# Performance work log

Measured on AMD Instinct MI355X. Metric: run time of the kernel, lower is better.

Reference implementation:

```python
import jax, jax.numpy as jnp
import numpy as np

N = 100000
E = 1600000
H = 2   # heads
C = 64  # per-head channels
NEG_SLOPE = 0.2


def setup_inputs() -> dict:
    key = jax.random.key(0)
    ks = jax.random.split(key, 12)
    s = 0.05
    return {
        "logits": jax.random.normal(ks[0], (N, 40), jnp.float32),
        "features": jax.random.normal(ks[1], (N, 256), jnp.float32),
        "edge_index": jax.random.randint(ks[2], (2, E), 0, N, jnp.int32),
        "W_feat": jax.random.normal(ks[3], (256, 128), jnp.float32) * s,
        "b_feat": jnp.zeros((128,), jnp.float32),
        "W0": jax.random.normal(ks[4], (168, 128), jnp.float32) * s,
        "att_src0": jax.random.normal(ks[5], (H, C), jnp.float32) * s,
        "att_dst0": jax.random.normal(ks[6], (H, C), jnp.float32) * s,
        "bias0": jnp.zeros((128,), jnp.float32),
        "W1": jax.random.normal(ks[7], (128, 128), jnp.float32) * s,
        "att_src1": jax.random.normal(ks[8], (H, C), jnp.float32) * s,
        "att_dst1": jax.random.normal(ks[9], (H, C), jnp.float32) * s,
        "bias1": jnp.zeros((128,), jnp.float32),
        "W_out": jax.random.normal(ks[10], (128, 40), jnp.float32) * s,
        "b_out": jnp.zeros((40,), jnp.float32),
    }


def gat_conv(x, src, dst, W, att_src, att_dst, bias):
    # x: [N, F_in] -> h: [N, H, C]
    h = (x @ W).reshape(N, H, C)
    a_src = (h * att_src).sum(-1)  # [N, H]
    a_dst = (h * att_dst).sum(-1)  # [N, H]
    # per-edge attention logits, leaky relu
    e = jax.nn.leaky_relu(a_src[src] + a_dst[dst], NEG_SLOPE)  # [E+N, H]
    # segment softmax over incoming edges of each dst node
    e_max = jax.ops.segment_max(e, dst, num_segments=N)
    e_exp = jnp.exp(e - e_max[dst])
    denom = jax.ops.segment_sum(e_exp, dst, num_segments=N)
    alpha = e_exp / (denom[dst] + 1e-16)  # [E+N, H]
    # weighted message aggregation (scatter-add)
    msg = h[src] * alpha[:, :, None]  # [E+N, H, C]
    out = jax.ops.segment_sum(msg, dst, num_segments=N)
    return out.reshape(N, H * C) + bias


def reference(logits, features, edge_index, W_feat, b_feat,
              W0, att_src0, att_dst0, bias0,
              W1, att_src1, att_dst1, bias1,
              W_out, b_out):
    # input assembly: [logits | proj(features)]
    x = jnp.concatenate([logits, features @ W_feat + b_feat], axis=-1)  # [N,168]
    # add self loops (PyG GATConv default add_self_loops=True)
    loops = jnp.arange(N, dtype=edge_index.dtype)
    src = jnp.concatenate([edge_index[0], loops])
    dst = jnp.concatenate([edge_index[1], loops])
    x = gat_conv(x, src, dst, W0, att_src0, att_dst0, bias0)
    x = jax.nn.relu(x)  # relu between conv layers (dropout=0 / eval)
    x = gat_conv(x, src, dst, W1, att_src1, att_dst1, bias1)
    return x @ W_out + b_out  # [N, 40]
```

## Files before the change

### kernel.cpp

```cpp
#include <hip/hip_runtime.h>

#define NN 100000
#define EE 1600000
#define NBUCK ((NN + 255) >> 8)
#define CHUNK 8192
#define NPBLK ((EE + CHUNK - 1) / CHUNK)

typedef __attribute__((ext_vector_type(8))) short short8_t;
typedef __attribute__((ext_vector_type(4))) float f32x4;

static __device__ inline unsigned short f2bf(float f) {
    unsigned int u = __float_as_uint(f);
    u += 0x7FFFu + ((u >> 16) & 1u);
    return (unsigned short)(u >> 16);
}
static __device__ inline float bf2f(unsigned short h) {
    return __uint_as_float(((unsigned int)h) << 16);
}
static __device__ inline float u2f(unsigned int u) { return __uint_as_float(u); }

__global__ __launch_bounds__(256) void part_count(const int* __restrict__ ei,
                                                  int* __restrict__ cnt) {
    __shared__ int h[NBUCK];
    for (int i = threadIdx.x; i < NBUCK; i += 256) h[i] = 0;
    __syncthreads();
    int e0 = blockIdx.x * CHUNK;
    int e1 = e0 + CHUNK; if (e1 > EE) e1 = EE;
    for (int e = e0 + threadIdx.x; e < e1; e += 256)
        atomicAdd(&h[ei[EE + e] >> 8], 1);
    __syncthreads();
    for (int i = threadIdx.x; i < NBUCK; i += 256)
        cnt[blockIdx.x * NBUCK + i] = h[i];
}

__global__ void part_scan(const int* __restrict__ cnt, int* __restrict__ base,
                          int* __restrict__ bbase) {
    __shared__ int tot[512];
    int b = threadIdx.x;
    int t = 0;
    if (b < NBUCK)
        for (int k = 0; k < NPBLK; ++k) t += cnt[k * NBUCK + b];
    tot[b] = t;
    __syncthreads();
    for (int off = 1; off < 512; off <<= 1) {
        int u = (b >= off) ? tot[b - off] : 0;
        __syncthreads();
        tot[b] += u;
        __syncthreads();
    }
    int excl = tot[b] - t;
    if (b < NBUCK) {
        bbase[b] = excl;
        int run = excl;
        for (int k = 0; k < NPBLK; ++k) {
            base[k * NBUCK + b] = run;
            run += cnt[k * NBUCK + b];
        }
    }
    if (b == 0) bbase[NBUCK] = EE;
}

__global__ __launch_bounds__(256) void part_scatter(const int* __restrict__ ei,
                                                    const int* __restrict__ base,
                                                    unsigned int* __restrict__ bbuf) {
    __shared__ int lcur[NBUCK];
    for (int i = threadIdx.x; i < NBUCK; i += 256)
        lcur[i] = base[blockIdx.x * NBUCK + i];
    __syncthreads();
    int e0 = blockIdx.x * CHUNK;
    int e1 = e0 + CHUNK; if (e1 > EE) e1 = EE;
    for (int e = e0 + threadIdx.x; e < e1; e += 256) {
        int s = ei[e], d = ei[EE + e];
        int pos = atomicAdd(&lcur[d >> 8], 1);
        bbuf[pos] = (unsigned int)s | ((unsigned int)(d & 255) << 24);
    }
}

__global__ __launch_bounds__(256) void csr_build(const unsigned int* __restrict__ bbuf,
                                                 const int* __restrict__ bbase,
                                                 int* __restrict__ row_ptr,
                                                 int* __restrict__ col) {
    __shared__ int hist[256];
    __shared__ int sc[256];
    __shared__ int lcur[256];
    int b = blockIdx.x;
    int t = threadIdx.x;
    int n0 = b << 8;
    int nCnt = NN - n0; if (nCnt > 256) nCnt = 256;
    int es = bbase[b], ee2 = bbase[b + 1];
    hist[t] = 0;
    __syncthreads();
    for (int i = es + t; i < ee2; i += 256)
        atomicAdd(&hist[bbuf[i] >> 24], 1);
    __syncthreads();
    int v = hist[t];
    sc[t] = v;
    __syncthreads();
    for (int off = 1; off < 256; off <<= 1) {
        int u = (t >= off) ? sc[t - off] : 0;
        __syncthreads();
        sc[t] += u;
        __syncthreads();
    }
    int excl = sc[t] - v;
    if (t < nCnt) row_ptr[n0 + t] = es + excl;
    if (b == 0 && t == 0) row_ptr[NN] = EE;
    lcur[t] = excl;
    __syncthreads();
    for (int i = es + t; i < ee2; i += 256) {
        unsigned int pk = bbuf[i];
        int lpos = atomicAdd(&lcur[pk >> 24], 1);
        col[es + lpos] = (int)(pk & 0x00FFFFFFu);
    }
}

__global__ void bsplit_kernel(const float* __restrict__ W, int ldw, int K, int N,
                              unsigned short* __restrict__ BThi,
                              unsigned short* __restrict__ BTlo,
                              int stride, int koff, int KPseg) {
    int k = blockIdx.x * 256 + threadIdx.x;
    int col = blockIdx.y;
    if (k >= KPseg) return;
    float v = (k < K && col < N) ? W[(size_t)k * ldw + col] : 0.f;
    unsigned short hi = f2bf(v);
    unsigned short lo = f2bf(v - bf2f(hi));
    BThi[(size_t)col * stride + koff + k] = hi;
    BTlo[(size_t)col * stride + koff + k] = lo;
}

__global__ void cvec_kernel(const float* __restrict__ b_feat,
                            const float* __restrict__ W0, float* __restrict__ cvec) {
    int j = threadIdx.x;
    float s = 0.f;
    for (int k = 0; k < 128; ++k) s += b_feat[k] * W0[(40 + k) * 128 + j];
    cvec[j] = s;
}

template <int OUTBF16, int AMODE, int ATTN, int NCT>
__global__ __launch_bounds__(256) void mfma_gemm_kernel(
    const void* __restrict__ A1v, int lda1, int K1, int KP1,
    const float* __restrict__ A2, int lda2, int K2,
    int M,
    const unsigned short* __restrict__ BThi, const unsigned short* __restrict__ BTlo,
    int bstride, int KPtot,
    void* __restrict__ Cout, int ldc, int Nact, const float* __restrict__ bias,
    const float* __restrict__ att_src, const float* __restrict__ att_dst,
    float* __restrict__ a_srcO, float* __restrict__ a_dstO)
{
    constexpr int ASZ = (AMODE == 0) ? 4096 : 2048;
    constexpr int BHALF = (NCT == 4) ? 4096 : 2048;
    constexpr int BHI_OFF = ASZ;
    constexpr int BLO_OFF = ASZ + BHALF;
    __shared__ __align__(16) unsigned short lds[ASZ + 2 * BHALF];

    const int t = threadIdx.x;
    const int w = t >> 6, lane = t & 63;
    const int row0 = blockIdx.x * 64;
    const int rbase = (w & 1) * 32;
    const int cbase = (NCT == 4) ? (w >> 1) * 64 : (w >> 1) * 32;

    f32x4 acc[2][NCT];
#pragma unroll
    for (int i = 0; i < 2; ++i)
#pragma unroll
        for (int j = 0; j < NCT; ++j) acc[i][j] = (f32x4){0.f, 0.f, 0.f, 0.f};

    const int arow = t >> 2;
    const int aslot = t & 3;
    const bool rowok = (row0 + arow) < M;
    const int aoff = arow * 32 + (((aslot ^ ((arow >> 1) & 3))) << 3);

    const int bc0 = t >> 2,         bs0 = t & 3;
    const int bc1 = (t + 256) >> 2, bs1 = (t + 256) & 3;
    const int bo0 = bc0 * 32 + ((bs0 ^ ((bc0 >> 1) & 3)) << 3);
    const int bo1 = bc1 * 32 + ((bs1 ^ ((bc1 >> 1) & 3)) << 3);

    float ra[8];
    short8_t rab;
    short8_t rbh0, rbl0, rbh1, rbl1;
    const short8_t zz = {0, 0, 0, 0, 0, 0, 0, 0};

#define LOADB_(k0_) {                                                     \
        size_t g0_ = (size_t)bc0 * bstride + (k0_) + bs0 * 8;             \
        rbh0 = *(const short8_t*)&BThi[g0_];                              \
        rbl0 = *(const short8_t*)&BTlo[g0_];                              \
        if (NCT == 4) {                                                   \
            size_t g1_ = (size_t)bc1 * bstride + (k0_) + bs1 * 8;         \
            rbh1 = *(const short8_t*)&BThi[g1_];                          \
            rbl1 = *(const short8_t*)&BTlo[g1_];                          \
        }                                                                 \
    }

#define LOADA_(k0_) {                                                     \
        if (AMODE == 1) {                                                 \
            int gk = (k0_) + aslot * 8;                                   \
            if (rowok && gk + 8 <= K1) {                                  \
                const unsigned short* Ab =                                \
                    (const unsigned short*)A1v + (size_t)(row0 + arow) * lda1; \
                rab = *(const short8_t*)&Ab[gk];                          \
            } else rab = zz;                                              \
        } else {                                                          \
            const float* Asrc; int gk, Klim;                              \
            if ((k0_) < KP1) {                                            \
                Asrc = (const float*)A1v + (size_t)(row0 + arow) * lda1;  \
                gk = (k0_) + aslot * 8; Klim = K1;                        \
            } else {                                                      \
                Asrc = A2 + (size_t)(row0 + arow) * lda2;                 \
                gk = (k0_) - KP1 + aslot * 8; Klim = K2;                  \
            }                                                             \
            if (rowok && gk + 8 <= Klim) {                                \
                float4 v0 = *(const float4*)(Asrc + gk);                  \
                float4 v1 = *(const float4*)(Asrc + gk + 4);              \
                ra[0] = v0.x; ra[1] = v0.y; ra[2] = v0.z; ra[3] = v0.w;   \
                ra[4] = v1.x; ra[5] = v1.y; ra[6] = v1.z; ra[7] = v1.w;   \
            } else {                                                      \
                for (int j_ = 0; j_ < 8; ++j_) ra[j_] = 0.f;              \
            }                                                             \
        }                                                                 \
    }

    LOADA_(0);
    LOADB_(0);

    for (int k0 = 0; k0 < KPtot; k0 += 32) {
        if (AMODE == 1) {
            *(short8_t*)&lds[aoff] = rab;
        } else if (AMODE == 2) {
            short8_t vh;
#pragma unroll
            for (int j = 0; j < 8; ++j) vh[j] = (short)f2bf(ra[j]);
            *(short8_t*)&lds[aoff] = vh;
        } else {
            short8_t vh, vl;
#pragma unroll
            for (int j = 0; j < 8; ++j) {
                unsigned short hi = f2bf(ra[j]);
                vh[j] = (short)hi;
                vl[j] = (short)f2bf(ra[j] - bf2f(hi));
            }
            *(short8_t*)&lds[aoff] = vh;
            *(short8_t*)&lds[2048 + aoff] = vl;
        }
        *(short8_t*)&lds[BHI_OFF + bo0] = rbh0;
        *(short8_t*)&lds[BLO_OFF + bo0] = rbl0;
        if (NCT == 4) {
            *(short8_t*)&lds[BHI_OFF + bo1] = rbh1;
            *(short8_t*)&lds[BLO_OFF + bo1] = rbl1;
        }
        __syncthreads();

        if (k0 + 32 < KPtot) {
            LOADA_(k0 + 32);
            LOADB_(k0 + 32);
        }

        short8_t Ah[2], Al[2], Bh[NCT], Bl[NCT];
        const int fslot = lane >> 4;
#pragma unroll
        for (int rt = 0; rt < 2; ++rt) {
            int r = rbase + rt * 16 + (lane & 15);
            int off = r * 32 + ((fslot ^ ((r >> 1) & 3)) << 3);
            Ah[rt] = *(const short8_t*)&lds[off];
            if (AMODE == 0) Al[rt] = *(const short8_t*)&lds[2048 + off];
        }
#pragma unroll
        for (int ct = 0; ct < NCT; ++ct) {
            int c = cbase + ct * 16 + (lane & 15);
            int off = c * 32 + ((fslot ^ ((c >> 1) & 3)) << 3);
            Bh[ct] = *(const short8_t*)&lds[BHI_OFF + off];
            Bl[ct] = *(const short8_t*)&lds[BLO_OFF + off];
        }
#pragma unroll
        for (int rt = 0; rt < 2; ++rt)
#pragma unroll
            for (int ct = 0; ct < NCT; ++ct) {
                acc[rt][ct] = __builtin_amdgcn_mfma_f32_16x16x32_bf16(Ah[rt], Bh[ct], acc[rt][ct], 0, 0, 0);
                acc[rt][ct] = __builtin_amdgcn_mfma_f32_16x16x32_bf16(Ah[rt], Bl[ct], acc[rt][ct], 0, 0, 0);
                if (AMODE == 0)
                    acc[rt][ct] = __builtin_amdgcn_mfma_f32_16x16x32_bf16(Al[rt], Bh[ct], acc[rt][ct], 0, 0, 0);
            }
        __syncthreads();
    }

#pragma unroll
    for (int rt = 0; rt < 2; ++rt) {
#pragma unroll
        for (int reg = 0; reg < 4; ++reg) {
            int r = row0 + rbase + rt * 16 + (lane >> 4) * 4 + reg;
            if (ATTN) {
                float ps = 0.f, pd = 0.f;
#pragma unroll
                for (int ct = 0; ct < NCT; ++ct) {
                    int c = cbase + ct * 16 + (lane & 15);
                    ps += acc[rt][ct][reg] * att_src[c];
                    pd += acc[rt][ct][reg] * att_dst[c];
                }
#pragma unroll
                for (int off = 1; off < 16; off <<= 1) {
                    ps += __shfl_xor(ps, off);
                    pd += __shfl_xor(pd, off);
                }
                if (r < M && (lane & 15) == 0) {
                    int head = w >> 1;
                    a_srcO[r * 2 + head] = ps;
                    a_dstO[r * 2 + head] = pd;
                }
            }
            if (r >= M) continue;
#pragma unroll
            for (int ct = 0; ct < NCT; ++ct) {
                int c = cbase + ct * 16 + (lane & 15);
                float v = acc[rt][ct][reg];
                if (OUTBF16) {
                    if (bias) v += bias[c];
                    ((unsigned short*)Cout)[(size_t)r * 128 + c] = f2bf(v);
                } else {
                    if (c < Nact) {
                        if (bias) v += bias[c];
                        ((float*)Cout)[(size_t)r * ldc + c] = v;
                    }
                }
            }
        }
    }
#undef LOADA_
#undef LOADB_
}

template <int RELU, int OUTBF16>
__global__ __launch_bounds__(256) void gat_agg_fused(
    const int* __restrict__ row_ptr, const int* __restrict__ col,
    const float* __restrict__ a_src, const float* __restrict__ a_dst,
    const unsigned short* __restrict__ hb,
    const float* __restrict__ bias, void* __restrict__ out)
{
    int wv = (blockIdx.x * 256 + threadIdx.x) >> 6;
    int lane = threadIdx.x & 63;
    int hl = lane >> 5;
    int l5 = lane & 31;
    int n = wv * 2 + hl;
    if (n >= NN) return;
    int hch = l5 >> 4;
    const uint2* h4 = (const uint2*)hb;

    float2 ad2 = ((const float2*)a_dst)[n];
    float adh = hch ? ad2.y : ad2.x;
    float2 as2 = ((const float2*)a_src)[n];
    float e0 = (hch ? as2.y : as2.x) + adh;
    e0 = e0 > 0.f ? e0 : 0.2f * e0;
    float w = __expf(e0);
    uint2 hv = h4[(size_t)n * 32 + l5];
    float a0 = w * u2f(hv.x << 16);
    float a1 = w * u2f(hv.x & 0xFFFF0000u);
    float a2 = w * u2f(hv.y << 16);
    float a3 = w * u2f(hv.y & 0xFFFF0000u);
    float den = w;

    int rs = row_ptr[n], re = row_ptr[n + 1];
    int deg = re - rs;
    int degO = __shfl(deg, lane ^ 32);
    int degm = deg > degO ? deg : degO;
    int nbm = (degm + 15) >> 4;

    for (int bi = 0; bi < nbm; ++bi) {
        int base = rs + bi * 16;
        int cnt = re - base;
        cnt = cnt < 0 ? 0 : (cnt > 16 ? 16 : cnt);
        int cntO = __shfl(cnt, lane ^ 32);
        int cntm = cnt > cntO ? cnt : cntO;
        int j16 = l5 & 15;
        int sL = 0;
        float wL = 0.f;
        if (j16 < cnt) {
            sL = col[base + j16];
            float2 as = ((const float2*)a_src)[sL];
            float tt = (hch ? as.y : as.x) + adh;
            tt = tt > 0.f ? tt : 0.2f * tt;
            wL = __expf(tt);
        }
        const int sb = hl << 5;
        const int wb = sb + (hch << 4);
        int i = 0;
        for (; i + 8 <= cntm; i += 8) {
            int s[8]; uint2 g[8]; float ws[8];
#pragma unroll
            for (int j = 0; j < 8; ++j) s[j] = __shfl(sL, sb + i + j);
#pragma unroll
            for (int j = 0; j < 8; ++j) g[j] = h4[(size_t)s[j] * 32 + l5];
#pragma unroll
            for (int j = 0; j < 8; ++j) ws[j] = __shfl(wL, wb + i + j);
#pragma unroll
            for (int j = 0; j < 8; ++j) {
                a0 += ws[j] * u2f(g[j].x << 16);
                a1 += ws[j] * u2f(g[j].x & 0xFFFF0000u);
                a2 += ws[j] * u2f(g[j].y << 16);
                a3 += ws[j] * u2f(g[j].y & 0xFFFF0000u);
                den += ws[j];
            }
        }
        for (; i + 4 <= cntm; i += 4) {
            int s[4]; uint2 g[4]; float ws[4];
#pragma unroll
            for (int j = 0; j < 4; ++j) s[j] = __shfl(sL, sb + i + j);
#pragma unroll
            for (int j = 0; j < 4; ++j) g[j] = h4[(size_t)s[j] * 32 + l5];
#pragma unroll
            for (int j = 0; j < 4; ++j) ws[j] = __shfl(wL, wb + i + j);
#pragma unroll
            for (int j = 0; j < 4; ++j) {
                a0 += ws[j] * u2f(g[j].x << 16);
                a1 += ws[j] * u2f(g[j].x & 0xFFFF0000u);
                a2 += ws[j] * u2f(g[j].y << 16);
                a3 += ws[j] * u2f(g[j].y & 0xFFFF0000u);
                den += ws[j];
            }
        }
        for (; i < cntm; ++i) {
            int s = __shfl(sL, sb + i);
            float ws = __shfl(wL, wb + i);
            uint2 g = h4[(size_t)s * 32 + l5];
            a0 += ws * u2f(g.x << 16);
            a1 += ws * u2f(g.x & 0xFFFF0000u);
            a2 += ws * u2f(g.y << 16);
            a3 += ws * u2f(g.y & 0xFFFF0000u);
            den += ws;
        }
    }
    float inv = 1.f / (den + 1e-16f);
    float4 b4 = ((const float4*)bias)[l5];
    float o0 = a0 * inv + b4.x;
    float o1 = a1 * inv + b4.y;
    float o2 = a2 * inv + b4.z;
    float o3 = a3 * inv + b4.w;
    if (RELU) {
        o0 = fmaxf(o0, 0.f); o1 = fmaxf(o1, 0.f);
        o2 = fmaxf(o2, 0.f); o3 = fmaxf(o3, 0.f);
    }
    if (OUTBF16) {
        uint2 pk;
        pk.x = (unsigned int)f2bf(o0) | ((unsigned int)f2bf(o1) << 16);
        pk.y = (unsigned int)f2bf(o2) | ((unsigned int)f2bf(o3) << 16);
        ((uint2*)out)[(size_t)n * 32 + l5] = pk;
    } else {
        ((float4*)out)[(size_t)n * 32 + l5] = make_float4(o0, o1, o2, o3);
    }
}

extern "C" void kernel_launch(void* const* d_in, const int* in_sizes, int n_in,
                              void* d_out, int out_size, void* d_ws, size_t ws_size,
                              hipStream_t stream) {
    const float* logits   = (const float*)d_in[0];
    const float* features = (const float*)d_in[1];
    const int*   ei       = (const int*)d_in[2];
    const float* W_feat   = (const float*)d_in[3];
    const float* b_feat   = (const float*)d_in[4];
    const float* W0       = (const float*)d_in[5];
    const float* att_src0 = (const float*)d_in[6];
    const float* att_dst0 = (const float*)d_in[7];
    const float* bias0    = (const float*)d_in[8];
    const float* W1       = (const float*)d_in[9];
    const float* att_src1 = (const float*)d_in[10];
    const float* att_dst1 = (const float*)d_in[11];
    const float* bias1    = (const float*)d_in[12];
    const float* W_out    = (const float*)d_in[13];
    const float* b_out    = (const float*)d_in[14];
    float* out = (float*)d_out;

    float* agg    = (float*)d_ws;
    float* a_srcb = agg + (size_t)NN * 128;
    float* a_dstb = a_srcb + (size_t)NN * 2;
    float* Wc     = a_dstb + (size_t)NN * 2;
    float* cvec   = Wc + 256 * 128;
    unsigned short* hbuf = (unsigned short*)(cvec + 128);
    unsigned short* BT0hi = hbuf + (size_t)NN * 128;
    unsigned short* BT0lo = BT0hi + 128 * 320;
    unsigned short* BTbhi = BT0lo + 128 * 320;
    unsigned short* BTblo = BTbhi + 128 * 128;
    unsigned short* BT1hi = BTblo + 128 * 128;
    unsigned short* BT1lo = BT1hi + 128 * 128;
    unsigned short* BTohi = BT1lo + 128 * 128;
    unsigned short* BTolo = BTohi + 128 * 128;
    int* row_ptr = (int*)(BTolo + 128 * 128);
    int* colbuf  = row_ptr + NN + 1;
    int* cnt     = colbuf + EE;
    int* pbase   = cnt + NPBLK * NBUCK;
    int* bbase   = pbase + NPBLK * NBUCK;
    unsigned int* bbuf = (unsigned int*)agg;
    unsigned short* aggb = (unsigned short*)agg;

    dim3 blk(256);
    const int gemmGrid = (NN + 63) / 64;
    const int aggGrid = (NN / 2 + 3) / 4;

    part_count<<<dim3(NPBLK), blk, 0, stream>>>(ei, cnt);
    part_scan<<<dim3(1), dim3(512), 0, stream>>>(cnt, pbase, bbase);
    part_scatter<<<dim3(NPBLK), blk, 0, stream>>>(ei, pbase, bbuf);
    csr_build<<<dim3(NBUCK), blk, 0, stream>>>(bbuf, bbase, row_ptr, colbuf);

    bsplit_kernel<<<dim3(1, 128), blk, 0, stream>>>(W0, 128, 40, 128, BT0hi, BT0lo, 320, 0, 64);
    bsplit_kernel<<<dim3(1, 128), blk, 0, stream>>>(W0 + 40 * 128, 128, 128, 128, BTbhi, BTblo, 128, 0, 128);
    mfma_gemm_kernel<0, 0, 0, 4><<<dim3(4), blk, 0, stream>>>(
        W_feat, 128, 128, 128, nullptr, 0, 0, 256,
        BTbhi, BTblo, 128, 128, Wc, 128, 128, nullptr,
        nullptr, nullptr, nullptr, nullptr);
    cvec_kernel<<<dim3(1), dim3(128), 0, stream>>>(b_feat, W0, cvec);
    bsplit_kernel<<<dim3(1, 128), blk, 0, stream>>>(Wc, 128, 256, 128, BT0hi, BT0lo, 320, 64, 256);
    bsplit_kernel<<<dim3(1, 128), blk, 0, stream>>>(W1, 128, 128, 128, BT1hi, BT1lo, 128, 0, 128);
    bsplit_kernel<<<dim3(1, 128), blk, 0, stream>>>(W_out, 40, 128, 40, BTohi, BTolo, 128, 0, 128);

    mfma_gemm_kernel<1, 2, 1, 4><<<dim3(gemmGrid), blk, 0, stream>>>(
        logits, 40, 40, 64, features, 256, 256, NN,
        BT0hi, BT0lo, 320, 320, hbuf, 128, 128, cvec,
        att_src0, att_dst0, a_srcb, a_dstb);
    gat_agg_fused<1, 1><<<dim3(aggGrid), blk, 0, stream>>>(
        row_ptr, colbuf, a_srcb, a_dstb, hbuf, bias0, aggb);

    mfma_gemm_kernel<1, 1, 1, 4><<<dim3(gemmGrid), blk, 0, stream>>>(
        aggb, 128, 128, 128, nullptr, 0, 0, NN,
        BT1hi, BT1lo, 128, 128, hbuf, 128, 128, nullptr,
        att_src1, att_dst1, a_srcb, a_dstb);
    gat_agg_fused<0, 1><<<dim3(aggGrid), blk, 0, stream>>>(
        row_ptr, colbuf, a_srcb, a_dstb, hbuf, bias1, aggb);

    mfma_gemm_kernel<0, 1, 0, 2><<<dim3(gemmGrid), blk, 0, stream>>>(
        aggb, 128, 128, 128, nullptr, 0, 0, NN,
        BTohi, BTolo, 128, 128, out, 40, 40, b_out,
        nullptr, nullptr, nullptr, nullptr);
}
```

Before: 286.7 us.

## Merge preprocessing kernels into fewer launches and overlap CSR build with layer-0 GEMM

Turns the CSR partition, weight-split, cvec and small GEMM kernels into device bodies that are dispatched by block index inside four combined kernels. Independent work now shares one grid. Examples are edge counting with the weight splits, the scan with the W_feat GEMM, and the scatter with the Wc split. The CSR build also runs in the same launch as the first large GEMM. The goal is to cut the number of kernel launches and the gaps between them, and to let the CSR build overlap the layer-0 GEMM. The scan is rewritten for 256 threads using double buffering. The fused kernels now use a common shared-memory size, which may lower occupancy for some roles.

```diff
diff --git a/kernel.cpp b/kernel.cpp
--- a/kernel.cpp
+++ b/kernel.cpp
@@ -19,55 +19,69 @@
 }
 static __device__ inline float u2f(unsigned int u) { return __uint_as_float(u); }
 
-__global__ __launch_bounds__(256) void part_count(const int* __restrict__ ei,
-                                                  int* __restrict__ cnt) {
-    __shared__ int h[NBUCK];
+static __device__ void part_count_body(int bid, int* h, const int* __restrict__ ei,
+                                       int* __restrict__ cnt) {
     for (int i = threadIdx.x; i < NBUCK; i += 256) h[i] = 0;
     __syncthreads();
-    int e0 = blockIdx.x * CHUNK;
+    int e0 = bid * CHUNK;
     int e1 = e0 + CHUNK; if (e1 > EE) e1 = EE;
     for (int e = e0 + threadIdx.x; e < e1; e += 256)
         atomicAdd(&h[ei[EE + e] >> 8], 1);
     __syncthreads();
     for (int i = threadIdx.x; i < NBUCK; i += 256)
-        cnt[blockIdx.x * NBUCK + i] = h[i];
-}
-
-__global__ void part_scan(const int* __restrict__ cnt, int* __restrict__ base,
-                          int* __restrict__ bbase) {
-    __shared__ int tot[512];
-    int b = threadIdx.x;
-    int t = 0;
-    if (b < NBUCK)
-        for (int k = 0; k < NPBLK; ++k) t += cnt[k * NBUCK + b];
-    tot[b] = t;
-    __syncthreads();
+        cnt[bid * NBUCK + i] = h[i];
+}
+
+static __device__ void part_scan_body(int* S, const int* __restrict__ cnt,
+                                      int* __restrict__ base, int* __restrict__ bbase) {
+    int* A = S;
+    int* B = S + 512;
+    int t = threadIdx.x;
+    int totLoc[2];
+#pragma unroll
+    for (int q = 0; q < 2; ++q) {
+        int idx = t + q * 256;
+        int v = 0;
+        if (idx < NBUCK)
+            for (int k = 0; k < NPBLK; ++k) v += cnt[k * NBUCK + idx];
+        totLoc[q] = v;
+        A[idx] = v;
+    }
+    __syncthreads();
+    int* src = A;
+    int* dst = B;
     for (int off = 1; off < 512; off <<= 1) {
-        int u = (b >= off) ? tot[b - off] : 0;
+#pragma unroll
+        for (int q = 0; q < 2; ++q) {
+            int idx = t + q * 256;
+            dst[idx] = src[idx] + (idx >= off ? src[idx - off] : 0);
+        }
         __syncthreads();
-        tot[b] += u;
-        __syncthreads();
-    }
-    int excl = tot[b] - t;
-    if (b < NBUCK) {
-        bbase[b] = excl;
-        int run = excl;
-        for (int k = 0; k < NPBLK; ++k) {
-            base[k * NBUCK + b] = run;
-            run += cnt[k * NBUCK + b];
-        }
-    }
-    if (b == 0) bbase[NBUCK] = EE;
-}
-
-__global__ __launch_bounds__(256) void part_scatter(const int* __restrict__ ei,
-                                                    const int* __restrict__ base,
-                                                    unsigned int* __restrict__ bbuf) {
-    __shared__ int lcur[NBUCK];
+        int* tmp = src; src = dst; dst = tmp;
+    }
+#pragma unroll
+    for (int q = 0; q < 2; ++q) {
+        int idx = t + q * 256;
+        if (idx < NBUCK) {
+            int excl = src[idx] - totLoc[q];
+            bbase[idx] = excl;
+            int run = excl;
+            for (int k = 0; k < NPBLK; ++k) {
+                base[k * NBUCK + idx] = run;
+                run += cnt[k * NBUCK + idx];
+            }
+        }
+    }
+    if (t == 0) bbase[NBUCK] = EE;
+}
+
+static __device__ void part_scatter_body(int bid, int* lcur, const int* __restrict__ ei,
+                                         const int* __restrict__ base,
+                                         unsigned int* __restrict__ bbuf) {
     for (int i = threadIdx.x; i < NBUCK; i += 256)
-        lcur[i] = base[blockIdx.x * NBUCK + i];
-    __syncthreads();
-    int e0 = blockIdx.x * CHUNK;
+        lcur[i] = base[bid * NBUCK + i];
+    __syncthreads();
+    int e0 = bid * CHUNK;
     int e1 = e0 + CHUNK; if (e1 > EE) e1 = EE;
     for (int e = e0 + threadIdx.x; e < e1; e += 256) {
         int s = ei[e], d = ei[EE + e];
@@ -76,14 +90,12 @@
     }
 }
 
-__global__ __launch_bounds__(256) void csr_build(const unsigned int* __restrict__ bbuf,
-                                                 const int* __restrict__ bbase,
-                                                 int* __restrict__ row_ptr,
-                                                 int* __restrict__ col) {
-    __shared__ int hist[256];
-    __shared__ int sc[256];
-    __shared__ int lcur[256];
-    int b = blockIdx.x;
+static __device__ void csr_build_body(int b, int* S, const unsigned int* __restrict__ bbuf,
+                                      const int* __restrict__ bbase,
+                                      int* __restrict__ row_ptr, int* __restrict__ col) {
+    int* hist = S;
+    int* sc   = S + 256;
+    int* lcur = S + 512;
     int t = threadIdx.x;
     int n0 = b << 8;
     int nCnt = NN - n0; if (nCnt > 256) nCnt = 256;
@@ -114,12 +126,11 @@
     }
 }
 
-__global__ void bsplit_kernel(const float* __restrict__ W, int ldw, int K, int N,
-                              unsigned short* __restrict__ BThi,
-                              unsigned short* __restrict__ BTlo,
-                              int stride, int koff, int KPseg) {
-    int k = blockIdx.x * 256 + threadIdx.x;
-    int col = blockIdx.y;
+static __device__ void bsplit_body(int col, const float* __restrict__ W, int ldw, int K, int N,
+                                   unsigned short* __restrict__ BThi,
+                                   unsigned short* __restrict__ BTlo,
+                                   int stride, int koff, int KPseg) {
+    int k = threadIdx.x;
     if (k >= KPseg) return;
     float v = (k < K && col < N) ? W[(size_t)k * ldw + col] : 0.f;
     unsigned short hi = f2bf(v);
@@ -128,16 +139,17 @@
     BTlo[(size_t)col * stride + koff + k] = lo;
 }
 
-__global__ void cvec_kernel(const float* __restrict__ b_feat,
-                            const float* __restrict__ W0, float* __restrict__ cvec) {
+static __device__ void cvec_body(const float* __restrict__ b_feat,
+                                 const float* __restrict__ W0, float* __restrict__ cvec) {
     int j = threadIdx.x;
+    if (j >= 128) return;
     float s = 0.f;
     for (int k = 0; k < 128; ++k) s += b_feat[k] * W0[(40 + k) * 128 + j];
     cvec[j] = s;
 }
 
 template <int OUTBF16, int AMODE, int ATTN, int NCT>
-__global__ __launch_bounds__(256) void mfma_gemm_kernel(
+static __device__ void gemm_body(int gbid, unsigned short* lds,
     const void* __restrict__ A1v, int lda1, int K1, int KP1,
     const float* __restrict__ A2, int lda2, int K2,
     int M,
@@ -151,11 +163,10 @@
     constexpr int BHALF = (NCT == 4) ? 4096 : 2048;
     constexpr int BHI_OFF = ASZ;
     constexpr int BLO_OFF = ASZ + BHALF;
-    __shared__ __align__(16) unsigned short lds[ASZ + 2 * BHALF];
 
     const int t = threadIdx.x;
     const int w = t >> 6, lane = t & 63;
-    const int row0 = blockIdx.x * 64;
+    const int row0 = gbid * 64;
     const int rbase = (w & 1) * 32;
     const int cbase = (NCT == 4) ? (w >> 1) * 64 : (w >> 1) * 32;
 
@@ -327,6 +338,97 @@
 #undef LOADB_
 }
 
+__global__ __launch_bounds__(256) void prep1_kernel(
+    const int* __restrict__ ei, int* __restrict__ cnt,
+    const float* __restrict__ W0, const float* __restrict__ W1,
+    const float* __restrict__ W_out, const float* __restrict__ b_feat,
+    unsigned short* BT0hi, unsigned short* BT0lo,
+    unsigned short* BTbhi, unsigned short* BTblo,
+    unsigned short* BT1hi, unsigned short* BT1lo,
+    unsigned short* BTohi, unsigned short* BTolo,
+    float* __restrict__ cvec)
+{
+    __shared__ int h[NBUCK];
+    int bid = blockIdx.x;
+    if (bid < NPBLK) { part_count_body(bid, h, ei, cnt); return; }
+    bid -= NPBLK;
+    if (bid < 128) { bsplit_body(bid, W0, 128, 40, 128, BT0hi, BT0lo, 320, 0, 64); return; }
+    bid -= 128;
+    if (bid < 128) { bsplit_body(bid, W0 + 40 * 128, 128, 128, 128, BTbhi, BTblo, 128, 0, 128); return; }
+    bid -= 128;
+    if (bid < 128) { bsplit_body(bid, W1, 128, 128, 128, BT1hi, BT1lo, 128, 0, 128); return; }
+    bid -= 128;
+    if (bid < 128) { bsplit_body(bid, W_out, 40, 128, 40, BTohi, BTolo, 128, 0, 128); return; }
+    cvec_body(b_feat, W0, cvec);
+}
+
+__global__ __launch_bounds__(256) void prep2_kernel(
+    const int* __restrict__ cnt, int* __restrict__ pbase, int* __restrict__ bbase,
+    const float* __restrict__ W_feat,
+    const unsigned short* BTbhi, const unsigned short* BTblo,
+    float* __restrict__ Wc)
+{
+    __shared__ __align__(16) unsigned short smem[12288];
+    if (blockIdx.x == 0) {
+        part_scan_body((int*)smem, cnt, pbase, bbase);
+    } else {
+        gemm_body<0, 0, 0, 4>(blockIdx.x - 1, smem,
+            W_feat, 128, 128, 128, nullptr, 0, 0, 256,
+            BTbhi, BTblo, 128, 128, Wc, 128, 128, nullptr,
+            nullptr, nullptr, nullptr, nullptr);
+    }
+}
+
+__global__ __launch_bounds__(256) void prep3_kernel(
+    const int* __restrict__ ei, const int* __restrict__ pbase,
+    unsigned int* __restrict__ bbuf,
+    const float* __restrict__ Wc,
+    unsigned short* BT0hi, unsigned short* BT0lo)
+{
+    __shared__ int lcur[NBUCK];
+    if (blockIdx.x < NPBLK) {
+        part_scatter_body(blockIdx.x, lcur, ei, pbase, bbuf);
+    } else {
+        bsplit_body(blockIdx.x - NPBLK, Wc, 128, 256, 128, BT0hi, BT0lo, 320, 64, 256);
+    }
+}
+
+__global__ __launch_bounds__(256) void csr_gemm_kernel(
+    const unsigned int* __restrict__ bbuf, const int* __restrict__ bbase,
+    int* __restrict__ row_ptr, int* __restrict__ colbuf,
+    const float* __restrict__ logits, const float* __restrict__ features,
+    const unsigned short* BT0hi, const unsigned short* BT0lo,
+    unsigned short* __restrict__ hbuf, const float* __restrict__ cvec,
+    const float* __restrict__ att_src0, const float* __restrict__ att_dst0,
+    float* __restrict__ a_srcb, float* __restrict__ a_dstb)
+{
+    __shared__ __align__(16) unsigned short smem[10240];
+    if (blockIdx.x < NBUCK) {
+        csr_build_body(blockIdx.x, (int*)smem, bbuf, bbase, row_ptr, colbuf);
+    } else {
+        gemm_body<1, 2, 1, 4>(blockIdx.x - NBUCK, smem,
+            logits, 40, 40, 64, features, 256, 256, NN,
+            BT0hi, BT0lo, 320, 320, hbuf, 128, 128, cvec,
+            att_src0, att_dst0, a_srcb, a_dstb);
+    }
+}
+
+template <int OUTBF16, int AMODE, int ATTN, int NCT>
+__global__ __launch_bounds__(256) void gemm_kernel(
+    const void* __restrict__ A1v, int lda1, int K1, int KP1,
+    const float* __restrict__ A2, int lda2, int K2, int M,
+    const unsigned short* __restrict__ BThi, const unsigned short* __restrict__ BTlo,
+    int bstride, int KPtot,
+    void* __restrict__ Cout, int ldc, int Nact, const float* __restrict__ bias,
+    const float* __restrict__ att_src, const float* __restrict__ att_dst,
+    float* __restrict__ a_srcO, float* __restrict__ a_dstO)
+{
+    __shared__ __align__(16) unsigned short lds[((AMODE == 0) ? 4096 : 2048) + ((NCT == 4) ? 8192 : 4096)];
+    gemm_body<OUTBF16, AMODE, ATTN, NCT>(blockIdx.x, lds,
+        A1v, lda1, K1, KP1, A2, lda2, K2, M, BThi, BTlo, bstride, KPtot,
+        Cout, ldc, Nact, bias, att_src, att_dst, a_srcO, a_dstO);
+}
+
 template <int RELU, int OUTBF16>
 __global__ __launch_bounds__(256) void gat_agg_fused(
     const int* __restrict__ row_ptr, const int* __restrict__ col,
@@ -492,37 +594,30 @@
     const int gemmGrid = (NN + 63) / 64;
     const int aggGrid = (NN / 2 + 3) / 4;
 
-    part_count<<<dim3(NPBLK), blk, 0, stream>>>(ei, cnt);
-    part_scan<<<dim3(1), dim3(512), 0, stream>>>(cnt, pbase, bbase);
-    part_scatter<<<dim3(NPBLK), blk, 0, stream>>>(ei, pbase, bbuf);
-    csr_build<<<dim3(NBUCK), blk, 0, stream>>>(bbuf, bbase, row_ptr, colbuf);
-
-    bsplit_kernel<<<dim3(1, 128), blk, 0, stream>>>(W0, 128, 40, 128, BT0hi, BT0lo, 320, 0, 64);
-    bsplit_kernel<<<dim3(1, 128), blk, 0, stream>>>(W0 + 40 * 128, 128, 128, 128, BTbhi, BTblo, 128, 0, 128);
-    mfma_gemm_kernel<0, 0, 0, 4><<<dim3(4), blk, 0, stream>>>(
-        W_feat, 128, 128, 128, nullptr, 0, 0, 256,
-        BTbhi, BTblo, 128, 128, Wc, 128, 128, nullptr,
-        nullptr, nullptr, nullptr, nullptr);
-    cvec_kernel<<<dim3(1), dim3(128), 0, stream>>>(b_feat, W0, cvec);
-    bsplit_kernel<<<dim3(1, 128), blk, 0, stream>>>(Wc, 128, 256, 128, BT0hi, BT0lo, 320, 64, 256);
-    bsplit_kernel<<<dim3(1, 128), blk, 0, stream>>>(W1, 128, 128, 128, BT1hi, BT1lo, 128, 0, 128);
-    bsplit_kernel<<<dim3(1, 128), blk, 0, stream>>>(W_out, 40, 128, 40, BTohi, BTolo, 128, 0, 128);
-
-    mfma_gemm_kernel<1, 2, 1, 4><<<dim3(gemmGrid), blk, 0, stream>>>(
-        logits, 40, 40, 64, features, 256, 256, NN,
-        BT0hi, BT0lo, 320, 320, hbuf, 128, 128, cvec,
+    prep1_kernel<<<dim3(NPBLK + 4 * 128 + 1), blk, 0, stream>>>(
+        ei, cnt, W0, W1, W_out, b_feat,
+        BT0hi, BT0lo, BTbhi, BTblo, BT1hi, BT1lo, BTohi, BTolo, cvec);
+
+    prep2_kernel<<<dim3(5), blk, 0, stream>>>(cnt, pbase, bbase, W_feat, BTbhi, BTblo, Wc);
+
+    prep3_kernel<<<dim3(NPBLK + 128), blk, 0, stream>>>(ei, pbase, bbuf, Wc, BT0hi, BT0lo);
+
+    csr_gemm_kernel<<<dim3(NBUCK + gemmGrid), blk, 0, stream>>>(
+        bbuf, bbase, row_ptr, colbuf,
+        logits, features, BT0hi, BT0lo, hbuf, cvec,
         att_src0, att_dst0, a_srcb, a_dstb);
+
     gat_agg_fused<1, 1><<<dim3(aggGrid), blk, 0, stream>>>(
         row_ptr, colbuf, a_srcb, a_dstb, hbuf, bias0, aggb);
 
-    mfma_gemm_kernel<1, 1, 1, 4><<<dim3(gemmGrid), blk, 0, stream>>>(
+    gemm_kernel<1, 1, 1, 4><<<dim3(gemmGrid), blk, 0, stream>>>(
         aggb, 128, 128, 128, nullptr, 0, 0, NN,
         BT1hi, BT1lo, 128, 128, hbuf, 128, 128, nullptr,
         att_src1, att_dst1, a_srcb, a_dstb);
     gat_agg_fused<0, 1><<<dim3(aggGrid), blk, 0, stream>>>(
         row_ptr, colbuf, a_srcb, a_dstb, hbuf, bias1, aggb);
 
-    mfma_gemm_kernel<0, 1, 0, 2><<<dim3(gemmGrid), blk, 0, stream>>>(
+    gemm_kernel<0, 1, 0, 2><<<dim3(gemmGrid), blk, 0, stream>>>(
         aggb, 128, 128, 128, nullptr, 0, 0, NN,
         BTohi, BTolo, 128, 128, out, 40, 40, b_out,
         nullptr, nullptr, nullptr, nullptr);
```

Result: faster. 266.8 us (median of 2 runs) (-6.9%).
